# Kernel tuning notes

Hardware: AMD Instinct MI355X
Metric: run time of the kernel (lower is better)

The kernel has to match this reference:

```python
import jax, jax.numpy as jnp
import numpy as np

B, L, D = 8, 4096, 2048
E, TOPK, RANK = 8, 2, 8
ALPHA = 1.0 / RANK
LN_EPS = 1e-5


def setup_inputs() -> dict:
    key = jax.random.key(0)
    ks = jax.random.split(key, 7)
    return {
        "x": jax.random.normal(ks[0], (B, L, D), dtype=jnp.float32),
        "gate_w": jax.random.normal(ks[1], (E, D), dtype=jnp.float32) * 0.02,
        "gate_b": jax.random.normal(ks[2], (E,), dtype=jnp.float32) * 0.02,
        "A": jax.random.normal(ks[3], (E, RANK, D), dtype=jnp.float32) * 0.02,
        "Bw": jax.random.normal(ks[4], (E, D, RANK), dtype=jnp.float32) * 0.02,
        "gamma": 1.0 + 0.1 * jax.random.normal(ks[5], (D,), dtype=jnp.float32),
        "beta": 0.1 * jax.random.normal(ks[6], (D,), dtype=jnp.float32),
    }


def reference(x, gate_w, gate_b, A, Bw, gamma, beta):
    # pooled hidden state per sequence: [B, D]
    h = x.mean(axis=1)
    # router (eval mode: no jitter noise)
    logits = h @ gate_w.T + gate_b                 # [B, E]
    vals, idx = jax.lax.top_k(logits, TOPK)        # [B, k]
    w = jax.nn.softmax(vals, axis=-1)              # [B, k]

    # ---- auxiliary losses ----
    counts = jnp.sum(jax.nn.one_hot(idx.reshape(-1), E, dtype=logits.dtype), axis=0)
    f = counts / (logits.shape[0] * TOPK)          # fraction routed to each expert
    P = jax.nn.softmax(logits, axis=-1).mean(axis=0)
    load_balance = E * jnp.sum(f * P)
    z_loss = jnp.mean(jax.nn.logsumexp(logits, axis=-1) ** 2)
    p = f + 1e-8
    p = p / p.sum()
    renyi_loss = jnp.log(jnp.sum(p ** 2))          # -(log(sum p^2)/(1-2))*(-1)
    aux = 0.01 * load_balance + 0.001 * z_loss + 0.01 * renyi_loss

    # ---- sparse LoRA expert dispatch (gather selected experts, tiny rank-8 GEMMs) ----
    A_sel = A[idx]                                 # [B, k, r, D]
    B_sel = Bw[idx]                                # [B, k, D, r]
    t = jnp.einsum('bd,bkrd->bkr', h, A_sel)       # [B, k, r]
    expert_out = jnp.einsum('bkr,bkdr->bkd', t, B_sel)  # [B, k, D]
    delta = jnp.sum(w[..., None] * expert_out, axis=1) * ALPHA  # [B, D]

    # residual add + LayerNorm over feature dim
    y = x + delta[:, None, :]
    mu = y.mean(axis=-1, keepdims=True)
    var = y.var(axis=-1, keepdims=True)
    y = (y - mu) / jnp.sqrt(var + LN_EPS) * gamma + beta
    return y, aux
```

## Files before the change

### kernel.cpp

```cpp
#include <hip/hip_runtime.h>
#include <math.h>

#define NB 8
#define NL 4096
#define ND 2048
#define NE 8
#define KTOP 2
#define NR 8
#define ALPHA 0.125f
#define LN_EPS 1e-5f

#define GB 4
#define NG (NB / GB)
#define SPLIT_S 32
#define ROWS_PER_S (NL / SPLIT_S)
#define DSL 8

typedef float f32x4 __attribute__((ext_vector_type(4)));

__global__ __launch_bounds__(256) void kA_partial(const float* __restrict__ x,
                                                  float* __restrict__ partial, int g) {
    int bid = blockIdx.x;
    int b_local = bid >> 8;
    int rem = bid & 255;
    int s = rem >> 3, dsl = rem & 7;
    int b = g * GB + b_local;
    int c4 = threadIdx.x & 63;
    int rbase = threadIdx.x >> 6;
    const float* xp = x + ((size_t)(b * NL + s * ROWS_PER_S + rbase)) * ND
                        + dsl * 256 + c4 * 4;
    f32x4 acc = {0.f, 0.f, 0.f, 0.f};
#pragma unroll 8
    for (int i = 0; i < ROWS_PER_S / 4; ++i) {
        f32x4 v = *(const f32x4*)(xp + (size_t)(4 * i) * ND);
        acc += v;
    }
    __shared__ f32x4 lds[256];
    lds[threadIdx.x] = acc;
    __syncthreads();
    if (threadIdx.x < 64) {
        f32x4 r = lds[threadIdx.x] + lds[threadIdx.x + 64] +
                  lds[threadIdx.x + 128] + lds[threadIdx.x + 192];
        *(f32x4*)(partial + (size_t)(b_local * SPLIT_S + s) * ND + dsl * 256
                  + threadIdx.x * 4) = r;
    }
}

__global__ __launch_bounds__(256) void kB_router(const float* __restrict__ partial,
                                                 const float* __restrict__ gate_w,
                                                 const float* __restrict__ gate_b,
                                                 const float* __restrict__ A,
                                                 const float* __restrict__ Bw,
                                                 float* __restrict__ delta,
                                                 float* __restrict__ logits_out,
                                                 int* __restrict__ idx_out, int g) {
    __shared__ float sh_h[ND];
    __shared__ float sh_logits[NE];
    __shared__ float sh_t[KTOP * NR];
    __shared__ float sh_w[KTOP];
    __shared__ int sh_idx[KTOP];
    int b_local = blockIdx.x;
    int b = g * GB + b_local;
    int tid = threadIdx.x;

    for (int d4 = tid; d4 < ND / 4; d4 += 256) {
        f32x4 sum = {0.f, 0.f, 0.f, 0.f};
#pragma unroll
        for (int s = 0; s < SPLIT_S; ++s)
            sum += *(const f32x4*)(partial + (size_t)(b_local * SPLIT_S + s) * ND + d4 * 4);
        f32x4 r = sum * (1.0f / NL);
        *(f32x4*)(sh_h + d4 * 4) = r;
    }
    __syncthreads();

    {
        int e = tid >> 5, lane32 = tid & 31;
        const f32x4* gw = (const f32x4*)(gate_w + (size_t)e * ND);
        float p = 0.f;
#pragma unroll 4
        for (int d4 = lane32; d4 < ND / 4; d4 += 32) {
            f32x4 gv = gw[d4];
            f32x4 hv = *(const f32x4*)(sh_h + d4 * 4);
            p += gv.x * hv.x + gv.y * hv.y + gv.z * hv.z + gv.w * hv.w;
        }
        for (int off = 16; off; off >>= 1) p += __shfl_down(p, off);
        if (lane32 == 0) sh_logits[e] = p + gate_b[e];
    }
    __syncthreads();

    if (tid == 0) {
        float v1 = -1e30f; int e1 = 0;
        for (int e = 0; e < NE; ++e) if (sh_logits[e] > v1) { v1 = sh_logits[e]; e1 = e; }
        float v2 = -1e30f; int e2 = 0;
        for (int e = 0; e < NE; ++e) if (e != e1 && sh_logits[e] > v2) { v2 = sh_logits[e]; e2 = e; }
        float ex = expf(v2 - v1);
        float w1 = 1.0f / (1.0f + ex);
        sh_idx[0] = e1; sh_idx[1] = e2;
        sh_w[0] = w1; sh_w[1] = ex * w1;
        idx_out[b * KTOP] = e1; idx_out[b * KTOP + 1] = e2;
        for (int e = 0; e < NE; ++e) logits_out[b * NE + e] = sh_logits[e];
    }
    __syncthreads();

    {
        int grp = tid >> 4, lane16 = tid & 15;
        int k = grp >> 3, r = grp & 7;
        int e = sh_idx[k];
        const f32x4* ap = (const f32x4*)(A + ((size_t)e * NR + r) * ND);
        float p = 0.f;
#pragma unroll 4
        for (int d4 = lane16; d4 < ND / 4; d4 += 16) {
            f32x4 av = ap[d4];
            f32x4 hv = *(const f32x4*)(sh_h + d4 * 4);
            p += av.x * hv.x + av.y * hv.y + av.z * hv.z + av.w * hv.w;
        }
        for (int off = 8; off; off >>= 1) p += __shfl_down(p, off);
        if (lane16 == 0) sh_t[grp] = p;
    }
    __syncthreads();

    for (int dd = tid; dd < ND; dd += 256) {
        float acc = 0.f;
#pragma unroll
        for (int k = 0; k < KTOP; ++k) {
            int e = sh_idx[k];
            const f32x4* bw = (const f32x4*)(Bw + ((size_t)e * ND + dd) * NR);
            f32x4 w0 = bw[0], w1 = bw[1];
            float s = sh_t[k * NR + 0] * w0.x + sh_t[k * NR + 1] * w0.y +
                      sh_t[k * NR + 2] * w0.z + sh_t[k * NR + 3] * w0.w +
                      sh_t[k * NR + 4] * w1.x + sh_t[k * NR + 5] * w1.y +
                      sh_t[k * NR + 6] * w1.z + sh_t[k * NR + 7] * w1.w;
            acc += sh_w[k] * s;
        }
        delta[b * ND + dd] = acc * ALPHA;
    }
}

__global__ void k3_aux(const float* __restrict__ logits, const int* __restrict__ idxp,
                       float* __restrict__ aux_out) {
    if (threadIdx.x != 0 || blockIdx.x != 0) return;
    float counts[NE];
    for (int e = 0; e < NE; ++e) counts[e] = 0.f;
    for (int i = 0; i < NB * KTOP; ++i) counts[idxp[i]] += 1.f;
    float f[NE], P[NE];
    for (int e = 0; e < NE; ++e) { f[e] = counts[e] * (1.0f / (NB * KTOP)); P[e] = 0.f; }
    float z = 0.f;
    for (int b = 0; b < NB; ++b) {
        const float* lg = logits + b * NE;
        float m = lg[0];
        for (int e = 1; e < NE; ++e) m = fmaxf(m, lg[e]);
        float s = 0.f;
        for (int e = 0; e < NE; ++e) s += expf(lg[e] - m);
        float inv = 1.0f / s;
        for (int e = 0; e < NE; ++e) P[e] += expf(lg[e] - m) * inv;
        float lse = m + logf(s);
        z += lse * lse;
    }
    z *= (1.0f / NB);
    float lb = 0.f;
    for (int e = 0; e < NE; ++e) lb += f[e] * (P[e] * (1.0f / NB));
    lb *= (float)NE;
    float psum = 0.f;
    for (int e = 0; e < NE; ++e) psum += f[e] + 1e-8f;
    float s2 = 0.f;
    for (int e = 0; e < NE; ++e) { float p = (f[e] + 1e-8f) / psum; s2 += p * p; }
    float renyi = logf(s2);
    aux_out[0] = 0.01f * lb + 0.001f * z + 0.01f * renyi;
}

__global__ __launch_bounds__(256) void kC_ln(const float* __restrict__ x,
                                             const float* __restrict__ delta,
                                             const float* __restrict__ gamma,
                                             const float* __restrict__ beta,
                                             float* __restrict__ y, int g) {
    int b = g * GB + (blockIdx.x >> 12);
    size_t base = ((size_t)g * GB * NL + blockIdx.x) * ND;
    int tid = threadIdx.x;
    int d0 = tid * 8;

    float4 xa = *(const float4*)(x + base + d0);
    float4 xb = *(const float4*)(x + base + d0 + 4);
    float4 da = *(const float4*)(delta + (size_t)b * ND + d0);
    float4 db = *(const float4*)(delta + (size_t)b * ND + d0 + 4);
    float v[8] = {xa.x + da.x, xa.y + da.y, xa.z + da.z, xa.w + da.w,
                  xb.x + db.x, xb.y + db.y, xb.z + db.z, xb.w + db.w};
    float s = 0.f, ss = 0.f;
#pragma unroll
    for (int j = 0; j < 8; ++j) { s += v[j]; ss += v[j] * v[j]; }
    for (int off = 32; off; off >>= 1) { s += __shfl_down(s, off); ss += __shfl_down(ss, off); }

    __shared__ float red[2][4];
    __shared__ float stats[2];
    int wid = tid >> 6, lane = tid & 63;
    if (lane == 0) { red[0][wid] = s; red[1][wid] = ss; }
    __syncthreads();
    if (tid == 0) {
        float S = red[0][0] + red[0][1] + red[0][2] + red[0][3];
        float SS = red[1][0] + red[1][1] + red[1][2] + red[1][3];
        float mu = S * (1.0f / ND);
        float var = SS * (1.0f / ND) - mu * mu;
        stats[0] = mu;
        stats[1] = rsqrtf(var + LN_EPS);
    }
    __syncthreads();
    float mu = stats[0], rstd = stats[1];

    float4 ga = *(const float4*)(gamma + d0);
    float4 gb = *(const float4*)(gamma + d0 + 4);
    float4 ba = *(const float4*)(beta + d0);
    float4 bb = *(const float4*)(beta + d0 + 4);
    f32x4 oa, ob;
    oa.x = (v[0] - mu) * rstd * ga.x + ba.x;
    oa.y = (v[1] - mu) * rstd * ga.y + ba.y;
    oa.z = (v[2] - mu) * rstd * ga.z + ba.z;
    oa.w = (v[3] - mu) * rstd * ga.w + ba.w;
    ob.x = (v[4] - mu) * rstd * gb.x + bb.x;
    ob.y = (v[5] - mu) * rstd * gb.y + bb.y;
    ob.z = (v[6] - mu) * rstd * gb.z + bb.z;
    ob.w = (v[7] - mu) * rstd * gb.w + bb.w;
    __builtin_nontemporal_store(oa, (f32x4*)(y + base + d0));
    __builtin_nontemporal_store(ob, (f32x4*)(y + base + d0 + 4));
}

extern "C" void kernel_launch(void* const* d_in, const int* in_sizes, int n_in,
                              void* d_out, int out_size, void* d_ws, size_t ws_size,
                              hipStream_t stream) {
    const float* x      = (const float*)d_in[0];
    const float* gate_w = (const float*)d_in[1];
    const float* gate_b = (const float*)d_in[2];
    const float* A      = (const float*)d_in[3];
    const float* Bw     = (const float*)d_in[4];
    const float* gamma  = (const float*)d_in[5];
    const float* beta   = (const float*)d_in[6];
    float* y   = (float*)d_out;
    float* aux = y + (size_t)NB * NL * ND;

    float* partial = (float*)d_ws;
    float* delta   = partial + (size_t)GB * SPLIT_S * ND;
    float* logits  = delta + NB * ND;
    int*   idxp    = (int*)(logits + NB * NE);

    for (int g = 0; g < NG; ++g) {
        hipLaunchKernelGGL(kA_partial, dim3(GB * SPLIT_S * DSL), dim3(256), 0, stream,
                           x, partial, g);
        hipLaunchKernelGGL(kB_router, dim3(GB), dim3(256), 0, stream,
                           partial, gate_w, gate_b, A, Bw, delta, logits, idxp, g);
        hipLaunchKernelGGL(kC_ln, dim3(GB * NL), dim3(256), 0, stream,
                           x, delta, gamma, beta, y, g);
    }
    hipLaunchKernelGGL(k3_aux, dim3(1), dim3(64), 0, stream, logits, idxp, aux);
}
```

Measured before the change: 168.7 us.

## Drop batch grouping; use single-pass mean/router/LN with a wave-per-row persistent LayerNorm

Removes the two-group batch loop so the partial-mean, router and LayerNorm kernels each run once over all 8 sequences. The mean kernel now uses a 64-way sequence split with four independent accumulators. The LayerNorm kernel becomes persistent: one wave per row, gamma and beta held in registers, and the reduction done with xor shuffles and no LDS or block barrier. This cuts launch count and per-row synchronisation. The risk is that the whole 256 MB input is now streamed before the LN pass rereads it, so the reuse the grouped schedule got from the last-level cache may be lost.

```diff
diff --git a/kernel.cpp b/kernel.cpp
--- a/kernel.cpp
+++ b/kernel.cpp
@@ -9,41 +9,29 @@
 #define NR 8
 #define ALPHA 0.125f
 #define LN_EPS 1e-5f
-
-#define GB 4
-#define NG (NB / GB)
-#define SPLIT_S 32
-#define ROWS_PER_S (NL / SPLIT_S)
-#define DSL 8
+#define SPLIT 64
 
 typedef float f32x4 __attribute__((ext_vector_type(4)));
 
-__global__ __launch_bounds__(256) void kA_partial(const float* __restrict__ x,
-                                                  float* __restrict__ partial, int g) {
+__global__ __launch_bounds__(256) void k1_partial_mean(const float* __restrict__ x,
+                                                       float* __restrict__ partial) {
     int bid = blockIdx.x;
-    int b_local = bid >> 8;
-    int rem = bid & 255;
-    int s = rem >> 3, dsl = rem & 7;
-    int b = g * GB + b_local;
-    int c4 = threadIdx.x & 63;
-    int rbase = threadIdx.x >> 6;
-    const float* xp = x + ((size_t)(b * NL + s * ROWS_PER_S + rbase)) * ND
-                        + dsl * 256 + c4 * 4;
-    f32x4 acc = {0.f, 0.f, 0.f, 0.f};
-#pragma unroll 8
-    for (int i = 0; i < ROWS_PER_S / 4; ++i) {
-        f32x4 v = *(const f32x4*)(xp + (size_t)(4 * i) * ND);
-        acc += v;
-    }
-    __shared__ f32x4 lds[256];
-    lds[threadIdx.x] = acc;
-    __syncthreads();
-    if (threadIdx.x < 64) {
-        f32x4 r = lds[threadIdx.x] + lds[threadIdx.x + 64] +
-                  lds[threadIdx.x + 128] + lds[threadIdx.x + 192];
-        *(f32x4*)(partial + (size_t)(b_local * SPLIT_S + s) * ND + dsl * 256
-                  + threadIdx.x * 4) = r;
-    }
+    int half = bid & 1;
+    int b = (bid >> 1) & (NB - 1);
+    int s = bid >> 4;
+    const int lchunk = NL / SPLIT;
+    int d4 = half * 1024 + threadIdx.x * 4;
+    const float* xp = x + ((size_t)(b * NL + s * lchunk)) * ND + d4;
+    f32x4 a0 = {0.f, 0.f, 0.f, 0.f}, a1 = a0, a2 = a0, a3 = a0;
+    for (int i = 0; i < lchunk; i += 4) {
+        f32x4 v0 = *(const f32x4*)(xp + (size_t)(i + 0) * ND);
+        f32x4 v1 = *(const f32x4*)(xp + (size_t)(i + 1) * ND);
+        f32x4 v2 = *(const f32x4*)(xp + (size_t)(i + 2) * ND);
+        f32x4 v3 = *(const f32x4*)(xp + (size_t)(i + 3) * ND);
+        a0 += v0; a1 += v1; a2 += v2; a3 += v3;
+    }
+    f32x4 acc = (a0 + a1) + (a2 + a3);
+    *(f32x4*)(partial + ((size_t)(b * SPLIT + s)) * ND + d4) = acc;
 }
 
 __global__ __launch_bounds__(256) void kB_router(const float* __restrict__ partial,
@@ -53,22 +41,26 @@
                                                  const float* __restrict__ Bw,
                                                  float* __restrict__ delta,
                                                  float* __restrict__ logits_out,
-                                                 int* __restrict__ idx_out, int g) {
+                                                 int* __restrict__ idx_out) {
     __shared__ float sh_h[ND];
     __shared__ float sh_logits[NE];
     __shared__ float sh_t[KTOP * NR];
     __shared__ float sh_w[KTOP];
     __shared__ int sh_idx[KTOP];
-    int b_local = blockIdx.x;
-    int b = g * GB + b_local;
+    int b = blockIdx.x;
     int tid = threadIdx.x;
 
+    const float* pb = partial + (size_t)b * SPLIT * ND;
     for (int d4 = tid; d4 < ND / 4; d4 += 256) {
-        f32x4 sum = {0.f, 0.f, 0.f, 0.f};
-#pragma unroll
-        for (int s = 0; s < SPLIT_S; ++s)
-            sum += *(const f32x4*)(partial + (size_t)(b_local * SPLIT_S + s) * ND + d4 * 4);
-        f32x4 r = sum * (1.0f / NL);
+        f32x4 s0 = {0.f, 0.f, 0.f, 0.f}, s1 = s0, s2 = s0, s3 = s0;
+#pragma unroll 4
+        for (int s = 0; s < SPLIT; s += 4) {
+            s0 += *(const f32x4*)(pb + (size_t)(s + 0) * ND + d4 * 4);
+            s1 += *(const f32x4*)(pb + (size_t)(s + 1) * ND + d4 * 4);
+            s2 += *(const f32x4*)(pb + (size_t)(s + 2) * ND + d4 * 4);
+            s3 += *(const f32x4*)(pb + (size_t)(s + 3) * ND + d4 * 4);
+        }
+        f32x4 r = ((s0 + s1) + (s2 + s3)) * (1.0f / NL);
         *(f32x4*)(sh_h + d4 * 4) = r;
     }
     __syncthreads();
@@ -168,58 +160,52 @@
     aux_out[0] = 0.01f * lb + 0.001f * z + 0.01f * renyi;
 }
 
-__global__ __launch_bounds__(256) void kC_ln(const float* __restrict__ x,
+__global__ __launch_bounds__(256) void k4_ln(const float* __restrict__ x,
                                              const float* __restrict__ delta,
                                              const float* __restrict__ gamma,
                                              const float* __restrict__ beta,
-                                             float* __restrict__ y, int g) {
-    int b = g * GB + (blockIdx.x >> 12);
-    size_t base = ((size_t)g * GB * NL + blockIdx.x) * ND;
-    int tid = threadIdx.x;
-    int d0 = tid * 8;
-
-    float4 xa = *(const float4*)(x + base + d0);
-    float4 xb = *(const float4*)(x + base + d0 + 4);
-    float4 da = *(const float4*)(delta + (size_t)b * ND + d0);
-    float4 db = *(const float4*)(delta + (size_t)b * ND + d0 + 4);
-    float v[8] = {xa.x + da.x, xa.y + da.y, xa.z + da.z, xa.w + da.w,
-                  xb.x + db.x, xb.y + db.y, xb.z + db.z, xb.w + db.w};
-    float s = 0.f, ss = 0.f;
-#pragma unroll
-    for (int j = 0; j < 8; ++j) { s += v[j]; ss += v[j] * v[j]; }
-    for (int off = 32; off; off >>= 1) { s += __shfl_down(s, off); ss += __shfl_down(ss, off); }
-
-    __shared__ float red[2][4];
-    __shared__ float stats[2];
-    int wid = tid >> 6, lane = tid & 63;
-    if (lane == 0) { red[0][wid] = s; red[1][wid] = ss; }
-    __syncthreads();
-    if (tid == 0) {
-        float S = red[0][0] + red[0][1] + red[0][2] + red[0][3];
-        float SS = red[1][0] + red[1][1] + red[1][2] + red[1][3];
-        float mu = S * (1.0f / ND);
-        float var = SS * (1.0f / ND) - mu * mu;
-        stats[0] = mu;
-        stats[1] = rsqrtf(var + LN_EPS);
-    }
-    __syncthreads();
-    float mu = stats[0], rstd = stats[1];
-
-    float4 ga = *(const float4*)(gamma + d0);
-    float4 gb = *(const float4*)(gamma + d0 + 4);
-    float4 ba = *(const float4*)(beta + d0);
-    float4 bb = *(const float4*)(beta + d0 + 4);
-    f32x4 oa, ob;
-    oa.x = (v[0] - mu) * rstd * ga.x + ba.x;
-    oa.y = (v[1] - mu) * rstd * ga.y + ba.y;
-    oa.z = (v[2] - mu) * rstd * ga.z + ba.z;
-    oa.w = (v[3] - mu) * rstd * ga.w + ba.w;
-    ob.x = (v[4] - mu) * rstd * gb.x + bb.x;
-    ob.y = (v[5] - mu) * rstd * gb.y + bb.y;
-    ob.z = (v[6] - mu) * rstd * gb.z + bb.z;
-    ob.w = (v[7] - mu) * rstd * gb.w + bb.w;
-    __builtin_nontemporal_store(oa, (f32x4*)(y + base + d0));
-    __builtin_nontemporal_store(ob, (f32x4*)(y + base + d0 + 4));
+                                             float* __restrict__ y) {
+    int wave = blockIdx.x * 4 + (threadIdx.x >> 6);
+    int lane = threadIdx.x & 63;
+
+    f32x4 g[8], be[8];
+#pragma unroll
+    for (int j = 0; j < 8; ++j) {
+        g[j]  = *(const f32x4*)(gamma + (lane + 64 * j) * 4);
+        be[j] = *(const f32x4*)(beta  + (lane + 64 * j) * 4);
+    }
+
+    for (int row = wave; row < NB * NL; row += 4096) {
+        int b = row >> 12;
+        const f32x4* xp = (const f32x4*)(x + (size_t)row * ND);
+        const f32x4* dp = (const f32x4*)(delta + (size_t)b * ND);
+        f32x4 v[8];
+#pragma unroll
+        for (int j = 0; j < 8; ++j) v[j] = xp[lane + 64 * j];
+#pragma unroll
+        for (int j = 0; j < 8; ++j) v[j] += dp[lane + 64 * j];
+
+        float s = 0.f, ss = 0.f;
+#pragma unroll
+        for (int j = 0; j < 8; ++j) {
+            s  += v[j].x + v[j].y + v[j].z + v[j].w;
+            ss += v[j].x * v[j].x + v[j].y * v[j].y + v[j].z * v[j].z + v[j].w * v[j].w;
+        }
+        for (int off = 32; off; off >>= 1) {
+            s  += __shfl_xor(s, off);
+            ss += __shfl_xor(ss, off);
+        }
+        float mu = s * (1.0f / ND);
+        float var = ss * (1.0f / ND) - mu * mu;
+        float rstd = rsqrtf(var + LN_EPS);
+
+        f32x4* yp = (f32x4*)(y + (size_t)row * ND);
+#pragma unroll
+        for (int j = 0; j < 8; ++j) {
+            f32x4 o = (v[j] - mu) * rstd * g[j] + be[j];
+            __builtin_nontemporal_store(o, yp + lane + 64 * j);
+        }
+    }
 }
 
 extern "C" void kernel_launch(void* const* d_in, const int* in_sizes, int n_in,
@@ -236,17 +222,15 @@
     float* aux = y + (size_t)NB * NL * ND;
 
     float* partial = (float*)d_ws;
-    float* delta   = partial + (size_t)GB * SPLIT_S * ND;
+    float* delta   = partial + (size_t)NB * SPLIT * ND;
     float* logits  = delta + NB * ND;
     int*   idxp    = (int*)(logits + NB * NE);
 
-    for (int g = 0; g < NG; ++g) {
-        hipLaunchKernelGGL(kA_partial, dim3(GB * SPLIT_S * DSL), dim3(256), 0, stream,
-                           x, partial, g);
-        hipLaunchKernelGGL(kB_router, dim3(GB), dim3(256), 0, stream,
-                           partial, gate_w, gate_b, A, Bw, delta, logits, idxp, g);
-        hipLaunchKernelGGL(kC_ln, dim3(GB * NL), dim3(256), 0, stream,
-                           x, delta, gamma, beta, y, g);
-    }
+    hipLaunchKernelGGL(k1_partial_mean, dim3(SPLIT * NB * 2), dim3(256), 0, stream,
+                       x, partial);
+    hipLaunchKernelGGL(kB_router, dim3(NB), dim3(256), 0, stream,
+                       partial, gate_w, gate_b, A, Bw, delta, logits, idxp);
     hipLaunchKernelGGL(k3_aux, dim3(1), dim3(64), 0, stream, logits, idxp, aux);
-}
+    hipLaunchKernelGGL(k4_ln, dim3(1024), dim3(256), 0, stream,
+                       x, delta, gamma, beta, y);
+}
```

New measurement: 151.9 us. 1.11x faster.
